# Kernel optimization log

Measured on AMD Instinct MI355X. Metric: run time of the kernel, lower is better.

## Reference

```python
import math
import jax, jax.numpy as jnp
import numpy as np

B, L, D, H = 2, 2048, 512, 8
HD = D // H
PADDING_IDX = 0


def _sinusoid_table(num_embeddings, dim, padding_idx):
    # matches RelativeSinusoidalPositionalEmbedding.get_embedding
    half = dim // 2
    inv = math.log(10000.0) / (half - 1)
    freqs = jnp.exp(jnp.arange(half, dtype=jnp.float32) * (-inv))
    ang = jnp.arange(num_embeddings, dtype=jnp.float32)[:, None] * freqs[None, :]
    emb = jnp.concatenate([jnp.sin(ang), jnp.cos(ang)], axis=1)  # [N, dim]
    return emb.at[padding_idx].set(0.0)


def _rel_pos_embed(seq_len):
    # RelativeEmbedding.forward: init table size 513 (origin_shift=257); since
    # padding_idx + seq_len > 257 it regenerates with num_embeddings = 2*seq_len,
    # origin_shift = seq_len. All static at trace time.
    init_origin = 512 // 2 + 1
    if PADDING_IDX + seq_len > init_origin:
        num = (PADDING_IDX + seq_len) * 2
        origin = num // 2
    else:
        num = 512 + 1
        origin = init_origin
    table = _sinusoid_table(num, HD, PADDING_IDX)
    positions = jnp.arange(-seq_len, seq_len) + origin  # [2L]
    return table[positions]  # [2L, HD]


def _shift(BD):
    # [B,H,L,2L] -> [B,H,L,L], Transformer-XL relative shift
    b, h, l, _ = BD.shape
    BD = jnp.concatenate([BD, jnp.zeros((b, h, l, 1), BD.dtype)], axis=-1)
    BD = BD.reshape(b, h, -1, l)[:, :, :-1].reshape(b, h, l, -1)
    return BD[:, :, :, l:]


def setup_inputs() -> dict:
    key = jax.random.key(0)
    ks = jax.random.split(key, 7)
    s = 1.0 / math.sqrt(D)
    return {
        "q": jax.random.normal(ks[0], (B, L, D), jnp.float32),
        "k": jax.random.normal(ks[1], (B, L, D), jnp.float32),
        "mask": jnp.ones((B, L, L), jnp.int32),
        "Wq": jax.random.normal(ks[2], (D, D), jnp.float32) * s,
        "Wkv": jax.random.normal(ks[3], (2 * D, D), jnp.float32) * s,
        "Wr": jax.random.normal(ks[4], (HD, HD), jnp.float32) * (1.0 / math.sqrt(HD)),
        "r_r_bias": jax.random.normal(ks[5], (H, HD), jnp.float32) * 0.1,
        "r_w_bias": jax.random.normal(ks[6], (H, HD), jnp.float32) * 0.1,
    }


def reference(q, k, mask, Wq, Wkv, Wr, r_r_bias, r_w_bias):
    b, l, d = q.shape
    scale = math.sqrt(HD)

    pos = _rel_pos_embed(l)                # [2L, HD]
    r = pos @ Wr.T                          # [2L, HD]

    qp = q @ Wq.T                           # [B,L,D]
    kv = k @ Wkv.T                          # [B,L,2D]
    kk, vv = jnp.split(kv, 2, axis=-1)

    qh = qp.reshape(b, l, H, HD).transpose(0, 2, 1, 3)  # [B,H,L,HD]
    kh = kk.reshape(b, l, H, HD).transpose(0, 2, 1, 3)
    vh = vv.reshape(b, l, H, HD).transpose(0, 2, 1, 3)

    rw_head_q = qh + r_r_bias[None, :, None, :]
    AC = jnp.einsum('bnqd,bnkd->bnqk', rw_head_q, kh)        # [B,H,L,L]
    D_ = jnp.einsum('nd,ld->nl', r_w_bias, r)[None, :, None, :]  # [1,H,1,2L]
    B_ = jnp.einsum('bnqd,ld->bnql', qh, r)                  # [B,H,L,2L]
    BD = _shift(B_ + D_)                                      # [B,H,L,L]

    attn = (AC + BD) / scale
    attn = jnp.where(mask[:, None, :, :] == 0, -jnp.inf, attn)
    attn = jax.nn.softmax(attn, axis=-1)

    out = jnp.einsum('bnqk,bnkd->bnqd', attn, vh)
    out = out.transpose(0, 2, 1, 3).reshape(b, l, d)
    return (out, attn)
```

## Files before the change

kernel.cpp:

```cpp
#include <hip/hip_runtime.h>
#include <math.h>

#define NL 2048
#define N2L 4096

typedef __attribute__((ext_vector_type(8))) short bf16x8;
typedef __attribute__((ext_vector_type(4))) float f32x4;
#define MFMA(a,b,c) __builtin_amdgcn_mfma_f32_16x16x32_bf16((a),(b),(c),0,0,0)

#define BARRIER() do {                                        \
    __builtin_amdgcn_sched_barrier(0);                        \
    asm volatile("s_waitcnt lgkmcnt(0)" ::: "memory");        \
    __builtin_amdgcn_s_barrier();                             \
    __builtin_amdgcn_sched_barrier(0);                        \
  } while (0)

__device__ __forceinline__ unsigned short bf16_rne(float x){
  unsigned int u = __float_as_uint(x);
  u += 0x7FFFu + ((u>>16)&1u);
  return (unsigned short)(u>>16);
}
__device__ __forceinline__ float bf16_to_f(unsigned short h){
  return __uint_as_float(((unsigned int)h)<<16);
}

__global__ __launch_bounds__(256) void split_kernel(
    const float* __restrict__ q, const float* __restrict__ k,
    const float* __restrict__ Wq, const float* __restrict__ Wkv,
    unsigned short* __restrict__ qsh, unsigned short* __restrict__ qsl,
    unsigned short* __restrict__ ksh, unsigned short* __restrict__ ksl,
    unsigned short* __restrict__ wqh, unsigned short* __restrict__ wql,
    unsigned short* __restrict__ wkh, unsigned short* __restrict__ wkl) {
  const int C1 = 524288, C2 = 1048576, C3 = 1114112, C4 = 1245184;
  for (int i = blockIdx.x * blockDim.x + threadIdx.x; i < C4; i += gridDim.x * blockDim.x) {
    const float* src; unsigned short *dh, *dl; int j;
    if (i < C1)      { src = q;   dh = qsh; dl = qsl; j = i; }
    else if (i < C2) { src = k;   dh = ksh; dl = ksl; j = i - C1; }
    else if (i < C3) { src = Wq;  dh = wqh; dl = wql; j = i - C2; }
    else             { src = Wkv; dh = wkh; dl = wkl; j = i - C3; }
    float4 v = reinterpret_cast<const float4*>(src)[j];
    unsigned short h0 = bf16_rne(v.x), h1 = bf16_rne(v.y), h2 = bf16_rne(v.z), h3 = bf16_rne(v.w);
    unsigned short l0 = bf16_rne(v.x - bf16_to_f(h0));
    unsigned short l1 = bf16_rne(v.y - bf16_to_f(h1));
    unsigned short l2 = bf16_rne(v.z - bf16_to_f(h2));
    unsigned short l3 = bf16_rne(v.w - bf16_to_f(h3));
    reinterpret_cast<uint2*>(dh)[j] = make_uint2((unsigned)h0 | ((unsigned)h1 << 16),
                                                 (unsigned)h2 | ((unsigned)h3 << 16));
    reinterpret_cast<uint2*>(dl)[j] = make_uint2((unsigned)l0 | ((unsigned)l1 << 16),
                                                 (unsigned)l2 | ((unsigned)l3 << 16));
  }
}

__global__ void build_r_kernel(const float* __restrict__ Wr,
                               unsigned short* __restrict__ rh,
                               unsigned short* __restrict__ rl) {
  int n = blockIdx.x;
  int t = threadIdx.x;
  __shared__ float pos[64];
  float v = 0.f;
  if (n != 0) {
    int j = t & 31;
    float inv = logf(10000.f) * (1.0f / 31.0f);
    float freq = expf(-inv * (float)j);
    float ang = (float)n * freq;
    v = (t < 32) ? sinf(ang) : cosf(ang);
  }
  pos[t] = v;
  __syncthreads();
  float acc = 0.f;
  const float* wrow = Wr + t * 64;
  #pragma unroll
  for (int j = 0; j < 64; ++j) acc += pos[j] * wrow[j];
  unsigned short hh = bf16_rne(acc);
  rh[n * 64 + t] = hh;
  rl[n * 64 + t] = bf16_rne(acc - bf16_to_f(hh));
}

__global__ __launch_bounds__(256) void proj_kernel(
    const unsigned short* __restrict__ qsh, const unsigned short* __restrict__ qsl,
    const unsigned short* __restrict__ ksh, const unsigned short* __restrict__ ksl,
    const unsigned short* __restrict__ wqh, const unsigned short* __restrict__ wql,
    const unsigned short* __restrict__ wkh, const unsigned short* __restrict__ wkl,
    const float* __restrict__ rrb, const float* __restrict__ rwb,
    unsigned short* __restrict__ qAh, unsigned short* __restrict__ qAl,
    unsigned short* __restrict__ qBh, unsigned short* __restrict__ qBl,
    unsigned short* __restrict__ khh, unsigned short* __restrict__ khl,
    unsigned short* __restrict__ vTh, unsigned short* __restrict__ vTl) {
  int tid = threadIdx.x;
  int w = tid >> 6, lane = tid & 63, li = lane & 15, g = lane >> 4;
  int bx = blockIdx.x, by = blockIdx.y;
  f32x4 acc[4];
  #pragma unroll
  for (int i = 0; i < 4; ++i) { acc[i][0]=0.f; acc[i][1]=0.f; acc[i][2]=0.f; acc[i][3]=0.f; }

  if (by < 16) {
    int n0 = by * 64, m0 = bx * 64;
    const unsigned short* Xh = (n0 < 512) ? qsh : ksh;
    const unsigned short* Xl = (n0 < 512) ? qsl : ksl;
    const unsigned short* Wh = (n0 < 512) ? (wqh + (size_t)n0 * 512) : (wkh + (size_t)(n0 - 512) * 512);
    const unsigned short* Wl = (n0 < 512) ? (wql + (size_t)n0 * 512) : (wkl + (size_t)(n0 - 512) * 512);
    int rowm = m0 + 16 * w + li;
    for (int ks = 0; ks < 16; ++ks) {
      int d0 = ks * 32 + 8 * g;
      bf16x8 ah = *(const bf16x8*)(Xh + (size_t)rowm * 512 + d0);
      bf16x8 al = *(const bf16x8*)(Xl + (size_t)rowm * 512 + d0);
      #pragma unroll
      for (int nt = 0; nt < 4; ++nt) {
        bf16x8 bh_ = *(const bf16x8*)(Wh + (size_t)(16 * nt + li) * 512 + d0);
        bf16x8 bl_ = *(const bf16x8*)(Wl + (size_t)(16 * nt + li) * 512 + d0);
        acc[nt] = MFMA(ah, bh_, acc[nt]);
        acc[nt] = MFMA(al, bh_, acc[nt]);
        acc[nt] = MFMA(ah, bl_, acc[nt]);
      }
    }
    if (n0 < 512) {
      int h = n0 >> 6;
      #pragma unroll
      for (int nt = 0; nt < 4; ++nt) {
        int d = 16 * nt + li;
        float rrv = rrb[h * 64 + d], rwv = rwb[h * 64 + d];
        #pragma unroll
        for (int r = 0; r < 4; ++r) {
          int m = m0 + 16 * w + 4 * g + r;
          int b = m >> 11, lt = m & 2047;
          size_t base = (((size_t)(b * 8 + h)) * 2048 + lt) * 64 + d;
          float a1 = acc[nt][r] + rrv;
          unsigned short h1 = bf16_rne(a1);
          qAh[base] = h1; qAl[base] = bf16_rne(a1 - bf16_to_f(h1));
          float a2 = acc[nt][r] + rwv;
          unsigned short h2 = bf16_rne(a2);
          qBh[base] = h2; qBl[base] = bf16_rne(a2 - bf16_to_f(h2));
        }
      }
    } else {
      int h = (n0 - 512) >> 6;
      #pragma unroll
      for (int nt = 0; nt < 4; ++nt) {
        int d = 16 * nt + li;
        #pragma unroll
        for (int r = 0; r < 4; ++r) {
          int m = m0 + 16 * w + 4 * g + r;
          int b = m >> 11, lt = m & 2047;
          size_t base = (((size_t)(b * 8 + h)) * 2048 + lt) * 64 + d;
          unsigned short h1 = bf16_rne(acc[nt][r]);
          khh[base] = h1; khl[base] = bf16_rne(acc[nt][r] - bf16_to_f(h1));
        }
      }
    }
  } else {
    int fy = by - 16, m0 = bx * 64, f0 = fy * 64;
    const unsigned short* Ah = wkh + (size_t)(512 + f0 + 16 * w + li) * 512;
    const unsigned short* Al = wkl + (size_t)(512 + f0 + 16 * w + li) * 512;
    for (int ks = 0; ks < 16; ++ks) {
      int d0 = ks * 32 + 8 * g;
      bf16x8 ah = *(const bf16x8*)(Ah + d0);
      bf16x8 al = *(const bf16x8*)(Al + d0);
      #pragma unroll
      for (int nt = 0; nt < 4; ++nt) {
        bf16x8 bh_ = *(const bf16x8*)(ksh + (size_t)(m0 + 16 * nt + li) * 512 + d0);
        bf16x8 bl_ = *(const bf16x8*)(ksl + (size_t)(m0 + 16 * nt + li) * 512 + d0);
        acc[nt] = MFMA(ah, bh_, acc[nt]);
        acc[nt] = MFMA(al, bh_, acc[nt]);
        acc[nt] = MFMA(ah, bl_, acc[nt]);
      }
    }
    int h = fy;
    #pragma unroll
    for (int nt = 0; nt < 4; ++nt) {
      int m = m0 + 16 * nt + li;
      int b = m >> 11, lt = m & 2047;
      #pragma unroll
      for (int r = 0; r < 4; ++r) {
        int d = 16 * w + 4 * g + r;
        size_t base = (((size_t)(b * 8 + h)) * 64 + d) * 2048 + lt;
        unsigned short h1 = bf16_rne(acc[nt][r]);
        vTh[base] = h1; vTl[base] = bf16_rne(acc[nt][r] - bf16_to_f(h1));
      }
    }
  }
}

__global__ __launch_bounds__(256) void attn_kernel(
    const unsigned short* __restrict__ qAh, const unsigned short* __restrict__ qAl,
    const unsigned short* __restrict__ qBh, const unsigned short* __restrict__ qBl,
    const unsigned short* __restrict__ khh, const unsigned short* __restrict__ khl,
    const unsigned short* __restrict__ vTh, const unsigned short* __restrict__ vTl,
    const unsigned short* __restrict__ rh, const unsigned short* __restrict__ rl,
    const int* __restrict__ mask, float* __restrict__ outp, float* __restrict__ attnp,
    float* __restrict__ rlbuf) {
  __shared__ float Tlds[96 * 34];
  __shared__ float Slds[2048];
  __shared__ unsigned int Plds[2048];
  __shared__ float rlf[32];

  int tid = threadIdx.x;
  int w = tid >> 6, lane = tid & 63, li = lane & 15, g = lane >> 4;
  int qlc = tid >> 3, jc = tid & 7, kc = jc * 8;
  int q0 = blockIdx.x * 32;
  int bh = blockIdx.y, b = bh >> 3, h = bh & 7;
  const unsigned short* qAhp = qAh + (size_t)bh * 131072;
  const unsigned short* qAlp = qAl + (size_t)bh * 131072;
  const unsigned short* qBhp = qBh + (size_t)bh * 131072;
  const unsigned short* qBlp = qBl + (size_t)bh * 131072;
  const unsigned short* khhp = khh + (size_t)bh * 131072;
  const unsigned short* khlp = khl + (size_t)bh * 131072;
  const unsigned short* vThp = vTh + (size_t)bh * 131072;
  const unsigned short* vTlp = vTl + (size_t)bh * 131072;
  const int* mrow = mask + (size_t)b * NL * NL + (size_t)(q0 + qlc) * NL;
  float* arow = attnp + (size_t)bh * NL * NL + (size_t)(q0 + qlc) * NL;

  bf16x8 fAh[2][2], fAl[2][2], fBh[2][2], fBl[2][2];
  #pragma unroll
  for (int nt = 0; nt < 2; ++nt)
    #pragma unroll
    for (int ks = 0; ks < 2; ++ks) {
      size_t o = (size_t)(q0 + 16 * nt + li) * 64 + 32 * ks + 8 * g;
      fAh[nt][ks] = *(const bf16x8*)(qAhp + o);
      fAl[nt][ks] = *(const bf16x8*)(qAlp + o);
      fBh[nt][ks] = *(const bf16x8*)(qBhp + o);
      fBl[nt][ks] = *(const bf16x8*)(qBlp + o);
    }

  unsigned int sread0 = (unsigned)(qlc * 256 + (((2 * jc) * 16) ^ ((qlc & 7) << 4)));
  unsigned int sread1 = (unsigned)(qlc * 256 + (((2 * jc + 1) * 16) ^ ((qlc & 7) << 4)));
  unsigned int woff = (unsigned)(qlc * 128 + ((kc * 2) ^ ((qlc & 7) << 4)));

  float lrun = 0.f;
  f32x4 accO[2];
  #pragma unroll
  for (int i = 0; i < 2; ++i) { accO[i][0]=0.f; accO[i][1]=0.f; accO[i][2]=0.f; accO[i][3]=0.f; }

  for (int kt = 0; kt < 32; ++kt) {
    int k0 = kt * 64;
    int4 mv1 = *(const int4*)(mrow + k0 + kc);
    int4 mv2 = *(const int4*)(mrow + k0 + kc + 4);
    bf16x8 vhf[2], vlf[2];
    #pragma unroll
    for (int ks = 0; ks < 2; ++ks) {
      size_t vo = (size_t)(16 * w + li) * NL + k0 + 32 * ks + 8 * g;
      vhf[ks] = *(const bf16x8*)(vThp + vo);
      vlf[ks] = *(const bf16x8*)(vTlp + vo);
    }
    int krow = k0 + 16 * w + li;
    f32x4 accS[2];
    #pragma unroll
    for (int i = 0; i < 2; ++i) { accS[i][0]=0.f; accS[i][1]=0.f; accS[i][2]=0.f; accS[i][3]=0.f; }
    #pragma unroll
    for (int ks = 0; ks < 2; ++ks) {
      size_t o = (size_t)krow * 64 + 32 * ks + 8 * g;
      bf16x8 ah = *(const bf16x8*)(khhp + o);
      bf16x8 al = *(const bf16x8*)(khlp + o);
      #pragma unroll
      for (int nt = 0; nt < 2; ++nt) {
        accS[nt] = MFMA(ah, fAh[nt][ks], accS[nt]);
        accS[nt] = MFMA(al, fAh[nt][ks], accS[nt]);
        accS[nt] = MFMA(ah, fAl[nt][ks], accS[nt]);
      }
    }
    int nlo = k0 - q0 + 2017;
    f32x4 accT[3];
    #pragma unroll
    for (int i = 0; i < 3; ++i) { accT[i][0]=0.f; accT[i][1]=0.f; accT[i][2]=0.f; accT[i][3]=0.f; }
    #pragma unroll
    for (int pp = 0; pp < 3; ++pp) {
      int pi = w * 3 + pp, jt = pi >> 1, ntp = pi & 1;
      int rrow = nlo + jt * 16 + li;
      if (rrow > 4095) rrow = 4095;
      #pragma unroll
      for (int ks = 0; ks < 2; ++ks) {
        size_t o = (size_t)rrow * 64 + 32 * ks + 8 * g;
        bf16x8 ah = *(const bf16x8*)(rh + o);
        bf16x8 al = *(const bf16x8*)(rl + o);
        accT[pp] = MFMA(ah, fBh[ntp][ks], accT[pp]);
        accT[pp] = MFMA(al, fBh[ntp][ks], accT[pp]);
        accT[pp] = MFMA(ah, fBl[ntp][ks], accT[pp]);
      }
    }
    #pragma unroll
    for (int pp = 0; pp < 3; ++pp) {
      int pi = w * 3 + pp, jt = pi >> 1, ntp = pi & 1;
      #pragma unroll
      for (int r = 0; r < 4; ++r)
        Tlds[(jt * 16 + 4 * g + r) * 34 + ntp * 16 + li] = accT[pp][r];
    }
    BARRIER();
    #pragma unroll
    for (int nt = 0; nt < 2; ++nt) {
      int ql_ = 16 * nt + li;
      float sv[4];
      #pragma unroll
      for (int r = 0; r < 4; ++r) {
        int kl = 16 * w + 4 * g + r;
        sv[r] = (accS[nt][r] + Tlds[(kl - ql_ + 31) * 34 + ql_]) * 0.125f;
      }
      unsigned int so = (unsigned)(ql_ * 256 + (((4 * w + g) * 16) ^ ((ql_ & 7) << 4)));
      *(float4*)((char*)Slds + so) = make_float4(sv[0], sv[1], sv[2], sv[3]);
    }
    BARRIER();
    float4 sa = *(const float4*)((const char*)Slds + sread0);
    float4 sb = *(const float4*)((const char*)Slds + sread1);
    float p0 = mv1.x ? __expf(sa.x) : 0.f;
    float p1 = mv1.y ? __expf(sa.y) : 0.f;
    float p2 = mv1.z ? __expf(sa.z) : 0.f;
    float p3 = mv1.w ? __expf(sa.w) : 0.f;
    float p4 = mv2.x ? __expf(sb.x) : 0.f;
    float p5 = mv2.y ? __expf(sb.y) : 0.f;
    float p6 = mv2.z ? __expf(sb.z) : 0.f;
    float p7 = mv2.w ? __expf(sb.w) : 0.f;
    *(float4*)(arow + k0 + kc) = make_float4(p0, p1, p2, p3);
    *(float4*)(arow + k0 + kc + 4) = make_float4(p4, p5, p6, p7);
    float ts = p0 + p1 + p2 + p3 + p4 + p5 + p6 + p7;
    ts += __shfl_xor(ts, 1);
    ts += __shfl_xor(ts, 2);
    ts += __shfl_xor(ts, 4);
    lrun += ts;
    unsigned short h0 = bf16_rne(p0), h1 = bf16_rne(p1), h2 = bf16_rne(p2), h3 = bf16_rne(p3);
    unsigned short h4 = bf16_rne(p4), h5 = bf16_rne(p5), h6 = bf16_rne(p6), h7 = bf16_rne(p7);
    unsigned short e0 = bf16_rne(p0 - bf16_to_f(h0)), e1 = bf16_rne(p1 - bf16_to_f(h1));
    unsigned short e2 = bf16_rne(p2 - bf16_to_f(h2)), e3 = bf16_rne(p3 - bf16_to_f(h3));
    unsigned short e4 = bf16_rne(p4 - bf16_to_f(h4)), e5 = bf16_rne(p5 - bf16_to_f(h5));
    unsigned short e6 = bf16_rne(p6 - bf16_to_f(h6)), e7 = bf16_rne(p7 - bf16_to_f(h7));
    *(uint4*)((char*)Plds + woff) =
        make_uint4((unsigned)h0 | ((unsigned)h1 << 16), (unsigned)h2 | ((unsigned)h3 << 16),
                   (unsigned)h4 | ((unsigned)h5 << 16), (unsigned)h6 | ((unsigned)h7 << 16));
    *(uint4*)((char*)Plds + 4096 + woff) =
        make_uint4((unsigned)e0 | ((unsigned)e1 << 16), (unsigned)e2 | ((unsigned)e3 << 16),
                   (unsigned)e4 | ((unsigned)e5 << 16), (unsigned)e6 | ((unsigned)e7 << 16));
    BARRIER();
    #pragma unroll
    for (int ks = 0; ks < 2; ++ks) {
      #pragma unroll
      for (int nt = 0; nt < 2; ++nt) {
        unsigned int ro = (unsigned)((16 * nt + li) * 128 + (((32 * ks + 8 * g) * 2) ^ ((li & 7) << 4)));
        bf16x8 ph = *(const bf16x8*)((const char*)Plds + ro);
        bf16x8 pl = *(const bf16x8*)((const char*)Plds + 4096 + ro);
        accO[nt] = MFMA(vhf[ks], ph, accO[nt]);
        accO[nt] = MFMA(vlf[ks], ph, accO[nt]);
        accO[nt] = MFMA(vhf[ks], pl, accO[nt]);
      }
    }
    BARRIER();
  }

  if (jc == 0) {
    float rv = 1.0f / lrun;
    rlf[qlc] = rv;
    rlbuf[(size_t)bh * NL + q0 + qlc] = rv;
  }
  BARRIER();
  float r0 = rlf[li], r1 = rlf[16 + li];
  #pragma unroll
  for (int nt = 0; nt < 2; ++nt) {
    float rn = nt ? r1 : r0;
    int qg = q0 + 16 * nt + li;
    int d = 16 * w + 4 * g;
    *(float4*)(outp + ((size_t)b * NL + qg) * 512 + h * 64 + d) =
        make_float4(accO[nt][0] * rn, accO[nt][1] * rn, accO[nt][2] * rn, accO[nt][3] * rn);
  }
}

__global__ __launch_bounds__(256) void rescale_kernel(
    const float* __restrict__ rlbuf, float* __restrict__ attnp) {
  int row = blockIdx.x;
  int bh = blockIdx.y;
  float rv = rlbuf[(size_t)bh * NL + row];
  float* ap = attnp + ((size_t)bh * NL + row) * NL + threadIdx.x * 8;
  float4 a = *(float4*)ap;
  float4 b2 = *(float4*)(ap + 4);
  *(float4*)ap = make_float4(a.x * rv, a.y * rv, a.z * rv, a.w * rv);
  *(float4*)(ap + 4) = make_float4(b2.x * rv, b2.y * rv, b2.z * rv, b2.w * rv);
}

extern "C" void kernel_launch(void* const* d_in, const int* in_sizes, int n_in,
                              void* d_out, int out_size, void* d_ws, size_t ws_size,
                              hipStream_t stream) {
  const float* q    = (const float*)d_in[0];
  const float* k    = (const float*)d_in[1];
  const int*   mask = (const int*)d_in[2];
  const float* Wq   = (const float*)d_in[3];
  const float* Wkv  = (const float*)d_in[4];
  const float* Wr   = (const float*)d_in[5];
  const float* rrb  = (const float*)d_in[6];
  const float* rwb  = (const float*)d_in[7];

  float* outp  = (float*)d_out;
  float* attnp = outp + (size_t)2 * NL * 512;

  unsigned short* W = (unsigned short*)d_ws;
  const size_t RHI = 0,            RLO = RHI + 262144;
  const size_t QSH = RLO + 262144, QSL = QSH + 2097152;
  const size_t KSH = QSL + 2097152, KSL = KSH + 2097152;
  const size_t WQH = KSL + 2097152, WQL = WQH + 262144;
  const size_t WKH = WQL + 262144,  WKL = WKH + 524288;
  const size_t QAH = WKL + 524288,  QAL = QAH + 2097152;
  const size_t QBH = QAL + 2097152, QBL = QBH + 2097152;
  const size_t KHH = QBL + 2097152, KHL = KHH + 2097152;
  const size_t VTH = KHL + 2097152, VTL = VTH + 2097152;
  const size_t RLB = VTL + 2097152;
  float* rlbuf = (float*)(W + RLB);

  hipLaunchKernelGGL(split_kernel, dim3(1024), dim3(256), 0, stream,
                     q, k, Wq, Wkv, W+QSH, W+QSL, W+KSH, W+KSL, W+WQH, W+WQL, W+WKH, W+WKL);
  hipLaunchKernelGGL(build_r_kernel, dim3(N2L), dim3(64), 0, stream, Wr, W+RHI, W+RLO);
  hipLaunchKernelGGL(proj_kernel, dim3(64, 24), dim3(256), 0, stream,
                     W+QSH, W+QSL, W+KSH, W+KSL, W+WQH, W+WQL, W+WKH, W+WKL, rrb, rwb,
                     W+QAH, W+QAL, W+QBH, W+QBL, W+KHH, W+KHL, W+VTH, W+VTL);
  hipLaunchKernelGGL(attn_kernel, dim3(64, 16), dim3(256), 0, stream,
                     W+QAH, W+QAL, W+QBH, W+QBL, W+KHH, W+KHL, W+VTH, W+VTL,
                     W+RHI, W+RLO, mask, outp, attnp, rlbuf);
  hipLaunchKernelGGL(rescale_kernel, dim3(NL, 16), dim3(256), 0, stream,
                     rlbuf, attnp);
}
```

Baseline: 570.2 us.

## Split attention key range across two blocks and combine partial outputs

Splits the key loop of the attention kernel into two halves handled by separate blocks (split-K), doubling the grid to raise occupancy and parallelism. Partial unnormalized outputs and row sums go to workspace, and a new combine kernel sums and normalizes them. It also raises wave priority around the MFMA sections, merges the T and P shared buffers to cut LDS use, and shifts the relative-position row offset so the clamp can be dropped. The cost is an extra kernel launch plus extra global traffic for the partials.

```diff
diff --git a/kernel.cpp b/kernel.cpp
--- a/kernel.cpp
+++ b/kernel.cpp
@@ -186,18 +186,18 @@
     const unsigned short* __restrict__ khh, const unsigned short* __restrict__ khl,
     const unsigned short* __restrict__ vTh, const unsigned short* __restrict__ vTl,
     const unsigned short* __restrict__ rh, const unsigned short* __restrict__ rl,
-    const int* __restrict__ mask, float* __restrict__ outp, float* __restrict__ attnp,
-    float* __restrict__ rlbuf) {
-  __shared__ float Tlds[96 * 34];
+    const int* __restrict__ mask, float* __restrict__ attnp,
+    float* __restrict__ oPart, float* __restrict__ rlbuf) {
+  __shared__ float TPbuf[3264];
   __shared__ float Slds[2048];
-  __shared__ unsigned int Plds[2048];
-  __shared__ float rlf[32];
+
+  float* Tlds = TPbuf;
 
   int tid = threadIdx.x;
   int w = tid >> 6, lane = tid & 63, li = lane & 15, g = lane >> 4;
   int qlc = tid >> 3, jc = tid & 7, kc = jc * 8;
   int q0 = blockIdx.x * 32;
-  int bh = blockIdx.y, b = bh >> 3, h = bh & 7;
+  int y = blockIdx.y, kh = y & 1, bh = y >> 1, b = bh >> 3;
   const unsigned short* qAhp = qAh + (size_t)bh * 131072;
   const unsigned short* qAlp = qAl + (size_t)bh * 131072;
   const unsigned short* qBhp = qBh + (size_t)bh * 131072;
@@ -230,7 +230,8 @@
   #pragma unroll
   for (int i = 0; i < 2; ++i) { accO[i][0]=0.f; accO[i][1]=0.f; accO[i][2]=0.f; accO[i][3]=0.f; }
 
-  for (int kt = 0; kt < 32; ++kt) {
+  int kt0 = kh * 16;
+  for (int kt = kt0; kt < kt0 + 16; ++kt) {
     int k0 = kt * 64;
     int4 mv1 = *(const int4*)(mrow + k0 + kc);
     int4 mv2 = *(const int4*)(mrow + k0 + kc + 4);
@@ -245,6 +246,7 @@
     f32x4 accS[2];
     #pragma unroll
     for (int i = 0; i < 2; ++i) { accS[i][0]=0.f; accS[i][1]=0.f; accS[i][2]=0.f; accS[i][3]=0.f; }
+    __builtin_amdgcn_s_setprio(1);
     #pragma unroll
     for (int ks = 0; ks < 2; ++ks) {
       size_t o = (size_t)krow * 64 + 32 * ks + 8 * g;
@@ -257,7 +259,7 @@
         accS[nt] = MFMA(ah, fAl[nt][ks], accS[nt]);
       }
     }
-    int nlo = k0 - q0 + 2017;
+    int nlo = k0 - q0 + 2016;
     f32x4 accT[3];
     #pragma unroll
     for (int i = 0; i < 3; ++i) { accT[i][0]=0.f; accT[i][1]=0.f; accT[i][2]=0.f; accT[i][3]=0.f; }
@@ -265,7 +267,6 @@
     for (int pp = 0; pp < 3; ++pp) {
       int pi = w * 3 + pp, jt = pi >> 1, ntp = pi & 1;
       int rrow = nlo + jt * 16 + li;
-      if (rrow > 4095) rrow = 4095;
       #pragma unroll
       for (int ks = 0; ks < 2; ++ks) {
         size_t o = (size_t)rrow * 64 + 32 * ks + 8 * g;
@@ -276,6 +277,7 @@
         accT[pp] = MFMA(ah, fBl[ntp][ks], accT[pp]);
       }
     }
+    __builtin_amdgcn_s_setprio(0);
     #pragma unroll
     for (int pp = 0; pp < 3; ++pp) {
       int pi = w * 3 + pp, jt = pi >> 1, ntp = pi & 1;
@@ -291,7 +293,7 @@
       #pragma unroll
       for (int r = 0; r < 4; ++r) {
         int kl = 16 * w + 4 * g + r;
-        sv[r] = (accS[nt][r] + Tlds[(kl - ql_ + 31) * 34 + ql_]) * 0.125f;
+        sv[r] = (accS[nt][r] + Tlds[(kl - ql_ + 32) * 34 + ql_]) * 0.125f;
       }
       unsigned int so = (unsigned)(ql_ * 256 + (((4 * w + g) * 16) ^ ((ql_ & 7) << 4)));
       *(float4*)((char*)Slds + so) = make_float4(sv[0], sv[1], sv[2], sv[3]);
@@ -320,50 +322,59 @@
     unsigned short e2 = bf16_rne(p2 - bf16_to_f(h2)), e3 = bf16_rne(p3 - bf16_to_f(h3));
     unsigned short e4 = bf16_rne(p4 - bf16_to_f(h4)), e5 = bf16_rne(p5 - bf16_to_f(h5));
     unsigned short e6 = bf16_rne(p6 - bf16_to_f(h6)), e7 = bf16_rne(p7 - bf16_to_f(h7));
-    *(uint4*)((char*)Plds + woff) =
+    *(uint4*)((char*)TPbuf + woff) =
         make_uint4((unsigned)h0 | ((unsigned)h1 << 16), (unsigned)h2 | ((unsigned)h3 << 16),
                    (unsigned)h4 | ((unsigned)h5 << 16), (unsigned)h6 | ((unsigned)h7 << 16));
-    *(uint4*)((char*)Plds + 4096 + woff) =
+    *(uint4*)((char*)TPbuf + 4096 + woff) =
         make_uint4((unsigned)e0 | ((unsigned)e1 << 16), (unsigned)e2 | ((unsigned)e3 << 16),
                    (unsigned)e4 | ((unsigned)e5 << 16), (unsigned)e6 | ((unsigned)e7 << 16));
     BARRIER();
+    __builtin_amdgcn_s_setprio(1);
     #pragma unroll
     for (int ks = 0; ks < 2; ++ks) {
       #pragma unroll
       for (int nt = 0; nt < 2; ++nt) {
         unsigned int ro = (unsigned)((16 * nt + li) * 128 + (((32 * ks + 8 * g) * 2) ^ ((li & 7) << 4)));
-        bf16x8 ph = *(const bf16x8*)((const char*)Plds + ro);
-        bf16x8 pl = *(const bf16x8*)((const char*)Plds + 4096 + ro);
+        bf16x8 ph = *(const bf16x8*)((const char*)TPbuf + ro);
+        bf16x8 pl = *(const bf16x8*)((const char*)TPbuf + 4096 + ro);
         accO[nt] = MFMA(vhf[ks], ph, accO[nt]);
         accO[nt] = MFMA(vlf[ks], ph, accO[nt]);
         accO[nt] = MFMA(vhf[ks], pl, accO[nt]);
       }
     }
+    __builtin_amdgcn_s_setprio(0);
     BARRIER();
   }
 
-  if (jc == 0) {
-    float rv = 1.0f / lrun;
-    rlf[qlc] = rv;
-    rlbuf[(size_t)bh * NL + q0 + qlc] = rv;
-  }
-  BARRIER();
-  float r0 = rlf[li], r1 = rlf[16 + li];
+  if (jc == 0)
+    rlbuf[(size_t)kh * 32768 + (size_t)bh * 2048 + q0 + qlc] = lrun;
+  float* op = oPart + (size_t)kh * 2097152 + (size_t)bh * 131072;
   #pragma unroll
   for (int nt = 0; nt < 2; ++nt) {
-    float rn = nt ? r1 : r0;
     int qg = q0 + 16 * nt + li;
     int d = 16 * w + 4 * g;
-    *(float4*)(outp + ((size_t)b * NL + qg) * 512 + h * 64 + d) =
-        make_float4(accO[nt][0] * rn, accO[nt][1] * rn, accO[nt][2] * rn, accO[nt][3] * rn);
+    *(float4*)(op + (size_t)qg * 64 + d) =
+        make_float4(accO[nt][0], accO[nt][1], accO[nt][2], accO[nt][3]);
   }
+}
+
+__global__ __launch_bounds__(256) void combine_kernel(
+    const float* __restrict__ oPart, const float* __restrict__ rlbuf,
+    float* __restrict__ outp) {
+  int bh = blockIdx.y, b = bh >> 3, h = bh & 7;
+  int q = blockIdx.x * 4 + (threadIdx.x >> 6);
+  int d = threadIdx.x & 63;
+  size_t i0 = ((size_t)bh * 2048 + q) * 64 + d;
+  float l = rlbuf[(size_t)bh * 2048 + q] + rlbuf[32768 + (size_t)bh * 2048 + q];
+  float o = oPart[i0] + oPart[2097152 + i0];
+  outp[((size_t)b * 2048 + q) * 512 + h * 64 + d] = o / l;
 }
 
 __global__ __launch_bounds__(256) void rescale_kernel(
     const float* __restrict__ rlbuf, float* __restrict__ attnp) {
   int row = blockIdx.x;
   int bh = blockIdx.y;
-  float rv = rlbuf[(size_t)bh * NL + row];
+  float rv = 1.0f / (rlbuf[(size_t)bh * 2048 + row] + rlbuf[32768 + (size_t)bh * 2048 + row]);
   float* ap = attnp + ((size_t)bh * NL + row) * NL + threadIdx.x * 8;
   float4 a = *(float4*)ap;
   float4 b2 = *(float4*)(ap + 4);
@@ -398,6 +409,7 @@
   const size_t VTH = KHL + 2097152, VTL = VTH + 2097152;
   const size_t RLB = VTL + 2097152;
   float* rlbuf = (float*)(W + RLB);
+  float* oPart = (float*)(W + QSH);
 
   hipLaunchKernelGGL(split_kernel, dim3(1024), dim3(256), 0, stream,
                      q, k, Wq, Wkv, W+QSH, W+QSL, W+KSH, W+KSL, W+WQH, W+WQL, W+WKH, W+WKL);
@@ -405,9 +417,11 @@
   hipLaunchKernelGGL(proj_kernel, dim3(64, 24), dim3(256), 0, stream,
                      W+QSH, W+QSL, W+KSH, W+KSL, W+WQH, W+WQL, W+WKH, W+WKL, rrb, rwb,
                      W+QAH, W+QAL, W+QBH, W+QBL, W+KHH, W+KHL, W+VTH, W+VTL);
-  hipLaunchKernelGGL(attn_kernel, dim3(64, 16), dim3(256), 0, stream,
+  hipLaunchKernelGGL(attn_kernel, dim3(64, 32), dim3(256), 0, stream,
                      W+QAH, W+QAL, W+QBH, W+QBL, W+KHH, W+KHL, W+VTH, W+VTL,
-                     W+RHI, W+RLO, mask, outp, attnp, rlbuf);
+                     W+RHI, W+RLO, mask, attnp, oPart, rlbuf);
+  hipLaunchKernelGGL(combine_kernel, dim3(512, 16), dim3(256), 0, stream,
+                     oPart, rlbuf, outp);
   hipLaunchKernelGGL(rescale_kernel, dim3(NL, 16), dim3(256), 0, stream,
                      rlbuf, attnp);
 }
```

After: 596.2 us. 1.05x slower.
